# Kernel optimization log

Measured on AMD Instinct MI355X. Metric: run time of the kernel, lower is better.

Reference implementation:

```python
import jax, jax.numpy as jnp
import numpy as np
import math

L, H, E, D = 4, 8, 256, 32  # layers, heads, embed, head_dim
SCALE = 1.0 / math.sqrt(D)

def _ln(x, w, b, eps=1e-5):
    mu = jnp.mean(x, -1, keepdims=True)
    var = jnp.mean((x - mu) ** 2, -1, keepdims=True)
    return (x - mu) * jax.lax.rsqrt(var + eps) * w + b

def setup_inputs() -> dict:
    key = jax.random.key(0)
    ks = jax.random.split(key, 16)
    B, S, C = 32, 512, 512
    w = lambda k, sh: jax.random.normal(k, sh, jnp.float32) * 0.05
    return {
        'cnn_features': jax.random.normal(ks[0], (B, S, C), jnp.float32),
        'cnn_w': w(ks[1], (E, C)), 'cnn_b': jnp.zeros((E,), jnp.float32),
        'tok_emb': w(ks[2], (2, E)),
        'Wq': w(ks[3], (L, E, E)), 'bq': jnp.zeros((L, E), jnp.float32),
        'Wk': w(ks[4], (L, E, E)), 'bk': jnp.zeros((L, E), jnp.float32),
        'Wv': w(ks[5], (L, E, E)), 'bv': jnp.zeros((L, E), jnp.float32),
        'Wo': w(ks[6], (L, E, E)), 'bo': jnp.zeros((L, E), jnp.float32),
        'ln1_w': jnp.ones((L, E), jnp.float32), 'ln1_b': jnp.zeros((L, E), jnp.float32),
        'ln2_w': jnp.ones((L, E), jnp.float32), 'ln2_b': jnp.zeros((L, E), jnp.float32),
        'mlp_w1': w(ks[7], (L, 3 * E, E)), 'mlp_b1': jnp.zeros((L, 3 * E), jnp.float32),
        'mlp_w2': w(ks[8], (L, E, 3 * E)), 'mlp_b2': jnp.zeros((L, E), jnp.float32),
        'lnf_w': jnp.ones((E,), jnp.float32), 'lnf_b': jnp.zeros((E,), jnp.float32),
        'out_w1': w(ks[9], (2 * E, E)), 'out_b1': jnp.zeros((2 * E,), jnp.float32),
        'out_w2': w(ks[10], (C, 2 * E)), 'out_b2': jnp.zeros((C,), jnp.float32),
    }

def _forward(cnn_features, cnn_w, cnn_b, tok_emb, Wq, bq, Wk, bk, Wv, bv, Wo, bo,
             ln1_w, ln1_b, ln2_w, ln2_b, mlp_w1, mlp_b1, mlp_w2, mlp_b2,
             lnf_w, lnf_b, out_w1, out_b1, out_w2, out_b2):
    B, S, _ = cnn_features.shape
    # CNN feature projection + token-type embedding (all tokens type 0)
    x = cnn_features @ cnn_w.T + cnn_b + tok_emb[0]  # [B,S,E]
    for i in range(L):
        q = (x @ Wq[i].T + bq[i]).reshape(B, S, H, D).transpose(0, 2, 1, 3)
        k = (x @ Wk[i].T + bk[i]).reshape(B, S, H, D).transpose(0, 2, 1, 3)
        v = (x @ Wv[i].T + bv[i]).reshape(B, S, H, D).transpose(0, 2, 1, 3)
        scores = jnp.einsum('bhqd,bhkd->bhqk', q, k) * SCALE
        attn = jax.nn.softmax(scores, axis=-1)  # dropout = identity (eval)
        attended = jnp.einsum('bhqk,bhkd->bhqd', attn, v)
        attended = attended.transpose(0, 2, 1, 3).reshape(B, S, E)
        attn_out = attended @ Wo[i].T + bo[i]
        x = _ln(x + attn_out, ln1_w[i], ln1_b[i])
        h = jax.nn.gelu(x @ mlp_w1[i].T + mlp_b1[i], approximate=False)
        mlp_out = h @ mlp_w2[i].T + mlp_b2[i]
        x = _ln(x + mlp_out, ln2_w[i], ln2_b[i])
    x = _ln(x, lnf_w, lnf_b)
    h = jax.nn.gelu(x @ out_w1.T + out_b1, approximate=False)
    out = jax.nn.relu(h @ out_w2.T + out_b2)  # [B,S,cnn_feature_dim]
    return out

def reference(cnn_features, cnn_w, cnn_b, tok_emb, Wq, bq, Wk, bk, Wv, bv, Wo, bo,
              ln1_w, ln1_b, ln2_w, ln2_b, mlp_w1, mlp_b1, mlp_w2, mlp_b2,
              lnf_w, lnf_b, out_w1, out_b1, out_w2, out_b2):
    return _forward(cnn_features, cnn_w, cnn_b, tok_emb, Wq, bq, Wk, bk, Wv, bv, Wo, bo,
                    ln1_w, ln1_b, ln2_w, ln2_b, mlp_w1, mlp_b1, mlp_w2, mlp_b2,
                    lnf_w, lnf_b, out_w1, out_b1, out_w2, out_b2)
```

## Files before the change

### kernel.cpp

```cpp
#include <hip/hip_runtime.h>
#include <hip/hip_bf16.h>
#include <math.h>

#define B_SZ 32
#define S_SZ 512
#define C_SZ 512
#define E_SZ 256
#define H_SZ 8
#define D_SZ 32
#define L_SZ 4
#define N_TOK (B_SZ * S_SZ)
#define HID 768
#define MB (1048576)

typedef __attribute__((ext_vector_type(8))) short bf16x8;
typedef __attribute__((ext_vector_type(4))) float f32x4_t;

__device__ __forceinline__ float gelu_f(float x) {
    return 0.5f * x * (1.0f + erff(x * 0.70710678118654752f));
}

__device__ __forceinline__ ushort f2bf(float f) {
    uint u = __float_as_uint(f);
    return (ushort)((u + 0x7FFFu + ((u >> 16) & 1u)) >> 16);
}
__device__ __forceinline__ uint pack2(float a, float b) {
    __hip_bfloat162 h = __float22bfloat162_rn(make_float2(a, b));
    union { __hip_bfloat162 h; uint u; } c; c.h = h;
    return c.u;
}
__device__ __forceinline__ void unpack8(uint4 u, float* f) {
    f[0] = __uint_as_float((u.x & 0xFFFFu) << 16); f[1] = __uint_as_float(u.x & 0xFFFF0000u);
    f[2] = __uint_as_float((u.y & 0xFFFFu) << 16); f[3] = __uint_as_float(u.y & 0xFFFF0000u);
    f[4] = __uint_as_float((u.z & 0xFFFFu) << 16); f[5] = __uint_as_float(u.z & 0xFFFF0000u);
    f[6] = __uint_as_float((u.w & 0xFFFFu) << 16); f[7] = __uint_as_float(u.w & 0xFFFF0000u);
}

__device__ __forceinline__ void gload16(const ushort* g, ushort* l) {
    __builtin_amdgcn_global_load_lds(
        (const __attribute__((address_space(1))) void*)g,
        (__attribute__((address_space(3))) void*)l, 16, 0, 0);
}

__global__ __launch_bounds__(256)
void cvt_kernel(const float* __restrict__ src, ushort* __restrict__ dst)
{
    const int i = (blockIdx.x * 256 + threadIdx.x) * 8;
    const float4 a = *(const float4*)(src + i);
    const float4 b = *(const float4*)(src + i + 4);
    uint4 o;
    o.x = pack2(a.x, a.y); o.y = pack2(a.z, a.w);
    o.z = pack2(b.x, b.y); o.w = pack2(b.z, b.w);
    *(uint4*)(dst + i) = o;
}

__global__ __launch_bounds__(256)
void wqkv_cvt_kernel(const float* __restrict__ Wq, const float* __restrict__ Wk,
                     const float* __restrict__ Wv, ushort* __restrict__ dst)
{
    const int i = (blockIdx.x * 256 + threadIdx.x) * 8;
    const int layer = i / 196608;
    const int rem = i - layer * 196608;
    const int sub = rem >> 16, off = rem & 65535;
    const float* src = (sub == 0 ? Wq : sub == 1 ? Wk : Wv) + layer * 65536 + off;
    const float4 a = *(const float4*)src;
    const float4 b = *(const float4*)(src + 4);
    uint4 o;
    o.x = pack2(a.x, a.y); o.y = pack2(a.z, a.w);
    o.z = pack2(b.x, b.y); o.w = pack2(b.z, b.w);
    *(uint4*)(dst + i) = o;
}

__global__ __launch_bounds__(256)
void bqkv_kernel(const float* __restrict__ bq, const float* __restrict__ bk,
                 const float* __restrict__ bv, float* __restrict__ dst)
{
    const int idx = blockIdx.x * 256 + threadIdx.x;
    const int layer = idx / 768, j = idx % 768;
    float v = (j < 256) ? bq[layer * 256 + j]
            : (j < 512) ? bk[layer * 256 + j - 256]
                        : bv[layer * 256 + j - 512];
    dst[layer * 768 + j] = v;
}

template<int ACT, int EPI, bool OF, bool OB>
__global__ __launch_bounds__(256)
void gemm_bf16_kernel(const ushort* __restrict__ A, const ushort* __restrict__ W,
                      const float* __restrict__ bias, const float* __restrict__ bias2,
                      float* __restrict__ Cf, ushort* __restrict__ Cb,
                      ushort* __restrict__ Cb2, int M, int K, int F)
{
    __shared__ __align__(16) ushort As[2][128 * 64];
    __shared__ __align__(16) ushort Bs[2][64 * 64];
    const int tid = threadIdx.x;
    const int bm = blockIdx.x * 128, bn = blockIdx.y * 64;
    const int lane = tid & 63, w = tid >> 6;
    const int lr8 = lane >> 3, lseg = lane & 7;
    const int lsx = lseg ^ lr8;
    const int wm = w >> 1, wn = w & 1;
    const int fr = lane & 15, fk = lane >> 4;
    const int fx = fr & 7;
    f32x4_t acc[4][2] = {};

    const ushort* Ag = A + (size_t)(bm + w * 32 + lr8) * K + lsx * 8;
    const ushort* Wg = W + (size_t)(bn + w * 16 + lr8) * K + lsx * 8;

    #pragma unroll
    for (int q = 0; q < 4; ++q) gload16(Ag + (size_t)q * 8 * K, &As[0][(w * 32 + q * 8) * 64]);
    #pragma unroll
    for (int q = 0; q < 2; ++q) gload16(Wg + (size_t)q * 8 * K, &Bs[0][(w * 16 + q * 8) * 64]);
    __syncthreads();

    const int NT = K >> 6;
    int cur = 0;
    for (int t = 0; t < NT; ++t) {
        if (t + 1 < NT) {
            const size_t k0 = (size_t)(t + 1) << 6;
            #pragma unroll
            for (int q = 0; q < 4; ++q)
                gload16(Ag + (size_t)q * 8 * K + k0, &As[cur ^ 1][(w * 32 + q * 8) * 64]);
            #pragma unroll
            for (int q = 0; q < 2; ++q)
                gload16(Wg + (size_t)q * 8 * K + k0, &Bs[cur ^ 1][(w * 16 + q * 8) * 64]);
        }
        bf16x8 af[2][4], bw[2][2];
        #pragma unroll
        for (int kk = 0; kk < 2; ++kk) {
            const int rs = ((kk * 4 + fk) ^ fx) * 8;
            #pragma unroll
            for (int i = 0; i < 4; ++i)
                af[kk][i] = *(const bf16x8*)&As[cur][(wm * 64 + i * 16 + fr) * 64 + rs];
            #pragma unroll
            for (int j = 0; j < 2; ++j)
                bw[kk][j] = *(const bf16x8*)&Bs[cur][(wn * 32 + j * 16 + fr) * 64 + rs];
        }
        #pragma unroll
        for (int kk = 0; kk < 2; ++kk)
            #pragma unroll
            for (int i = 0; i < 4; ++i)
                #pragma unroll
                for (int j = 0; j < 2; ++j)
                    acc[i][j] = __builtin_amdgcn_mfma_f32_16x16x32_bf16(af[kk][i], bw[kk][j], acc[i][j], 0, 0, 0);
        __syncthreads();
        cur ^= 1;
    }

    #pragma unroll
    for (int j = 0; j < 2; ++j) {
        const int col = bn + wn * 32 + j * 16 + fr;
        float bb = bias[col];
        if (bias2) bb += bias2[col];
        #pragma unroll
        for (int i = 0; i < 4; ++i) {
            #pragma unroll
            for (int r = 0; r < 4; ++r) {
                const int row = bm + wm * 64 + i * 16 + fk * 4 + r;
                float t = acc[i][j][r] + bb;
                if (ACT == 1) t = gelu_f(t);
                if (ACT == 2) t = fmaxf(t, 0.0f);
                if (EPI == 1) {
                    const int b2 = row >> 9, s2 = row & 511;
                    if (col < 512) {
                        Cb[(size_t)row * 512 + col] = f2bf(t);
                    } else {
                        const int cc = col - 512;
                        Cb2[(size_t)(((b2 << 3) + (cc >> 5)) << 14) + ((cc & 31) << 9) + s2] = f2bf(t);
                    }
                } else {
                    if (OF) Cf[(size_t)row * F + col] = t;
                    if (OB) Cb[(size_t)row * F + col] = f2bf(t);
                }
            }
        }
    }
}

__global__ __launch_bounds__(512)
void attn_v4(const ushort* __restrict__ qk, const ushort* __restrict__ vt,
             ushort* __restrict__ out)
{
    __shared__ __align__(16) ushort Ks[512 * 40];
    __shared__ __align__(16) ushort Vs[32 * 520];
    const int bh = blockIdx.x;
    const int b = bh >> 3, h = bh & 7;
    const int tid = threadIdx.x;
    const int w = tid >> 6, lane = tid & 63;
    const int g = lane >> 4, c = lane & 15;

    #pragma unroll
    for (int i = 0; i < 4; ++i) {
        const int idx = tid + i * 512;
        const int kr = idx >> 2, seg = idx & 3;
        const uint4 kv = *(const uint4*)(qk + ((size_t)b * 512 + kr) * 512
                                         + 256 + h * 32 + seg * 8);
        const int p = (((kr >> 2) & 1) << 4) | (((kr >> 3) & 3) << 2) | (kr & 3);
        const int pos = (kr & ~31) | p;
        *(uint4*)&Ks[pos * 40 + seg * 8] = kv;
        const int dr = idx >> 6, vseg = idx & 63;
        const uint4 vv = *(const uint4*)(vt + (size_t)bh * 16384 + dr * 512 + vseg * 8);
        *(uint4*)&Vs[dr * 520 + vseg * 8] = vv;
    }

    bf16x8 qf[4];
    #pragma unroll
    for (int j = 0; j < 4; ++j) {
        const size_t qrow = (size_t)b * 512 + (j * 8 + w) * 16 + c;
        const uint4 qv = *(const uint4*)(qk + qrow * 512 + h * 32 + g * 8);
        float f[8]; unpack8(qv, f);
        const float scale = 0.17677669529663689f;
        union { uint u[4]; bf16x8 v; } qq;
        #pragma unroll
        for (int t = 0; t < 4; ++t) qq.u[t] = pack2(f[2*t] * scale, f[2*t+1] * scale);
        qf[j] = qq.v;
    }
    __syncthreads();

    const f32x4_t zz = {0.f, 0.f, 0.f, 0.f};
    #pragma unroll
    for (int j = 0; j < 4; ++j) {
        float m = -INFINITY, l = 0.f;
        f32x4_t o0 = zz, o1 = zz;
        for (int kt = 0; kt < 4; ++kt) {
            const int kbase = kt * 128;
            f32x4_t s[8];
            __builtin_amdgcn_s_setprio(1);
            #pragma unroll
            for (int kf = 0; kf < 8; ++kf) {
                const bf16x8 kfrag = *(const bf16x8*)&Ks[(kbase + kf * 16 + c) * 40 + g * 8];
                s[kf] = __builtin_amdgcn_mfma_f32_16x16x32_bf16(kfrag, qf[j], zz, 0, 0, 0);
            }
            __builtin_amdgcn_s_setprio(0);

            float mt = s[0][0];
            #pragma unroll
            for (int kf = 0; kf < 8; ++kf)
                #pragma unroll
                for (int r = 0; r < 4; ++r) mt = fmaxf(mt, s[kf][r]);
            mt = fmaxf(mt, __shfl_xor(mt, 16));
            mt = fmaxf(mt, __shfl_xor(mt, 32));
            const float mn = fmaxf(m, mt);
            const float corr = __expf(m - mn);
            m = mn;
            float lt = 0.f;
            #pragma unroll
            for (int kf = 0; kf < 8; ++kf)
                #pragma unroll
                for (int r = 0; r < 4; ++r) {
                    const float p = __expf(s[kf][r] - mn);
                    s[kf][r] = p; lt += p;
                }
            lt += __shfl_xor(lt, 16);
            lt += __shfl_xor(lt, 32);
            l = l * corr + lt;
            #pragma unroll
            for (int r = 0; r < 4; ++r) { o0[r] *= corr; o1[r] *= corr; }

            #pragma unroll
            for (int t = 0; t < 4; ++t) {
                union { uint u[4]; bf16x8 v; } pf;
                pf.u[0] = pack2(s[2*t][0],   s[2*t][1]);
                pf.u[1] = pack2(s[2*t][2],   s[2*t][3]);
                pf.u[2] = pack2(s[2*t+1][0], s[2*t+1][1]);
                pf.u[3] = pack2(s[2*t+1][2], s[2*t+1][3]);
                const bf16x8 va0 = *(const bf16x8*)&Vs[c * 520 + kbase + t * 32 + g * 8];
                const bf16x8 va1 = *(const bf16x8*)&Vs[(16 + c) * 520 + kbase + t * 32 + g * 8];
                __builtin_amdgcn_s_setprio(1);
                o0 = __builtin_amdgcn_mfma_f32_16x16x32_bf16(va0, pf.v, o0, 0, 0, 0);
                o1 = __builtin_amdgcn_mfma_f32_16x16x32_bf16(va1, pf.v, o1, 0, 0, 0);
                __builtin_amdgcn_s_setprio(0);
            }
        }

        const float inv = 1.0f / l;
        const size_t obase = ((size_t)b * 512 + (j * 8 + w) * 16 + c) * 256 + h * 32;
        ushort4 w0, w1;
        w0.x = f2bf(o0[0] * inv); w0.y = f2bf(o0[1] * inv);
        w0.z = f2bf(o0[2] * inv); w0.w = f2bf(o0[3] * inv);
        w1.x = f2bf(o1[0] * inv); w1.y = f2bf(o1[1] * inv);
        w1.z = f2bf(o1[2] * inv); w1.w = f2bf(o1[3] * inv);
        *(ushort4*)(out + obase + g * 4)      = w0;
        *(ushort4*)(out + obase + 16 + g * 4) = w1;
    }
}

__global__ __launch_bounds__(256)
void add_ln2_kernel(float* __restrict__ x, const float* __restrict__ resid,
                    const float* __restrict__ w, const float* __restrict__ b,
                    ushort* __restrict__ xb)
{
    const int lane = threadIdx.x & 63;
    const int wv = threadIdx.x >> 6;
    const size_t row = (size_t)blockIdx.x * 4 + wv;
    float4 val = *(const float4*)(x + row * E_SZ + lane * 4);
    if (resid) {
        const float4 r = *(const float4*)(resid + row * E_SZ + lane * 4);
        val.x += r.x; val.y += r.y; val.z += r.z; val.w += r.w;
    }
    float s  = val.x + val.y + val.z + val.w;
    float ss = val.x * val.x + val.y * val.y + val.z * val.z + val.w * val.w;
    #pragma unroll
    for (int off = 1; off < 64; off <<= 1) {
        s  += __shfl_xor(s, off, 64);
        ss += __shfl_xor(ss, off, 64);
    }
    const float mu  = s * (1.0f / 256.0f);
    const float var = ss * (1.0f / 256.0f) - mu * mu;
    const float rs  = rsqrtf(var + 1e-5f);
    const float4 wv4 = *(const float4*)(w + lane * 4);
    const float4 bv4 = *(const float4*)(b + lane * 4);
    float4 o;
    o.x = (val.x - mu) * rs * wv4.x + bv4.x;
    o.y = (val.y - mu) * rs * wv4.y + bv4.y;
    o.z = (val.z - mu) * rs * wv4.z + bv4.z;
    o.w = (val.w - mu) * rs * wv4.w + bv4.w;
    *(float4*)(x + row * E_SZ + lane * 4) = o;
    ushort4 ob;
    ob.x = f2bf(o.x); ob.y = f2bf(o.y); ob.z = f2bf(o.z); ob.w = f2bf(o.w);
    *(ushort4*)(xb + row * E_SZ + lane * 4) = ob;
}

extern "C" void kernel_launch(void* const* d_in, const int* in_sizes, int n_in,
                              void* d_out, int out_size, void* d_ws, size_t ws_size,
                              hipStream_t stream)
{
    const float* cnn   = (const float*)d_in[0];
    const float* cnn_w = (const float*)d_in[1];
    const float* cnn_b = (const float*)d_in[2];
    const float* tok   = (const float*)d_in[3];
    const float* Wq    = (const float*)d_in[4];
    const float* bq    = (const float*)d_in[5];
    const float* Wk    = (const float*)d_in[6];
    const float* bk    = (const float*)d_in[7];
    const float* Wv    = (const float*)d_in[8];
    const float* bv    = (const float*)d_in[9];
    const float* Wo    = (const float*)d_in[10];
    const float* bo    = (const float*)d_in[11];
    const float* ln1w  = (const float*)d_in[12];
    const float* ln1b  = (const float*)d_in[13];
    const float* ln2w  = (const float*)d_in[14];
    const float* ln2b  = (const float*)d_in[15];
    const float* mw1   = (const float*)d_in[16];
    const float* mb1   = (const float*)d_in[17];
    const float* mw2   = (const float*)d_in[18];
    const float* mb2   = (const float*)d_in[19];
    const float* lnfw  = (const float*)d_in[20];
    const float* lnfb  = (const float*)d_in[21];
    const float* ow1   = (const float*)d_in[22];
    const float* ob1   = (const float*)d_in[23];
    const float* ow2   = (const float*)d_in[24];
    const float* ob2   = (const float*)d_in[25];

    const int M = N_TOK;
    char* ws = (char*)d_ws;

    float*  x     = (float*)(ws + 0);
    ushort* xb    = (ushort*)(ws + 16 * MB);
    ushort* qkb   = (ushort*)(ws + 24 * MB);
    float*  resid = (float*)(ws + 24 * MB);
    ushort* cnnb  = (ushort*)(ws + 24 * MB);
    ushort* vt    = (ushort*)(ws + 40 * MB);
    ushort* ab_   = (ushort*)(ws + 48 * MB);
    ushort* hb_   = (ushort*)(ws + 40 * MB);
    ushort* wb    = (ushort*)(ws + 64 * MB);

    ushort* cnn_wb = wb;
    ushort* Wob    = wb + 131072;
    ushort* wqkv   = wb + 393216;
    ushort* mw1b   = wb + 1179648;
    ushort* mw2b   = wb + 1966080;
    ushort* ow1b   = wb + 2752512;
    ushort* ow2b   = wb + 2883584;
    float*  bqkv   = (float*)(ws + 64 * MB + 6291456);

    cvt_kernel<<<dim3(4096), dim3(256), 0, stream>>>(cnn, cnnb);
    cvt_kernel<<<dim3(64),  dim3(256), 0, stream>>>(cnn_w, cnn_wb);
    cvt_kernel<<<dim3(128), dim3(256), 0, stream>>>(Wo, Wob);
    cvt_kernel<<<dim3(384), dim3(256), 0, stream>>>(mw1, mw1b);
    cvt_kernel<<<dim3(384), dim3(256), 0, stream>>>(mw2, mw2b);
    cvt_kernel<<<dim3(64),  dim3(256), 0, stream>>>(ow1, ow1b);
    cvt_kernel<<<dim3(128), dim3(256), 0, stream>>>(ow2, ow2b);
    wqkv_cvt_kernel<<<dim3(384), dim3(256), 0, stream>>>(Wq, Wk, Wv, wqkv);
    bqkv_kernel<<<dim3(12), dim3(256), 0, stream>>>(bq, bk, bv, bqkv);

    gemm_bf16_kernel<0, 0, true, true><<<dim3(M / 128, E_SZ / 64), dim3(256), 0, stream>>>(
        cnnb, cnn_wb, cnn_b, tok, x, xb, nullptr, M, C_SZ, E_SZ);

    for (int i = 0; i < L_SZ; ++i) {
        gemm_bf16_kernel<0, 1, false, false><<<dim3(M / 128, HID / 64), dim3(256), 0, stream>>>(
            xb, wqkv + (size_t)i * 196608, bqkv + (size_t)i * 768, nullptr,
            nullptr, qkb, vt, M, E_SZ, HID);

        attn_v4<<<dim3(B_SZ * H_SZ), dim3(512), 0, stream>>>(qkb, vt, ab_);

        gemm_bf16_kernel<0, 0, true, false><<<dim3(M / 128, E_SZ / 64), dim3(256), 0, stream>>>(
            ab_, Wob + (size_t)i * 65536, bo + (size_t)i * E_SZ, nullptr,
            resid, nullptr, nullptr, M, E_SZ, E_SZ);
        add_ln2_kernel<<<dim3(M / 4), dim3(256), 0, stream>>>(
            x, resid, ln1w + (size_t)i * E_SZ, ln1b + (size_t)i * E_SZ, xb);

        gemm_bf16_kernel<1, 0, false, true><<<dim3(M / 128, HID / 64), dim3(256), 0, stream>>>(
            xb, mw1b + (size_t)i * HID * E_SZ, mb1 + (size_t)i * HID, nullptr,
            nullptr, hb_, nullptr, M, E_SZ, HID);
        gemm_bf16_kernel<0, 0, true, false><<<dim3(M / 128, E_SZ / 64), dim3(256), 0, stream>>>(
            hb_, mw2b + (size_t)i * E_SZ * HID, mb2 + (size_t)i * E_SZ, nullptr,
            resid, nullptr, nullptr, M, HID, E_SZ);
        add_ln2_kernel<<<dim3(M / 4), dim3(256), 0, stream>>>(
            x, resid, ln2w + (size_t)i * E_SZ, ln2b + (size_t)i * E_SZ, xb);
    }

    add_ln2_kernel<<<dim3(M / 4), dim3(256), 0, stream>>>(x, nullptr, lnfw, lnfb, xb);

    gemm_bf16_kernel<1, 0, false, true><<<dim3(M / 128, (2 * E_SZ) / 64), dim3(256), 0, stream>>>(
        xb, ow1b, ob1, nullptr, nullptr, hb_, nullptr, M, E_SZ, 2 * E_SZ);
    gemm_bf16_kernel<2, 0, true, false><<<dim3(M / 128, C_SZ / 64), dim3(256), 0, stream>>>(
        hb_, ow2b, ob2, nullptr, (float*)d_out, nullptr, nullptr, M, 2 * E_SZ, C_SZ);
}
```

Baseline: 578.8 us.

## Fuse residual add and LayerNorm into output-projection and MLP-down GEMMs

Adds a GEMM kernel in which each block owns a full 64x256 row tile, so it can add bias and residual and compute LayerNorm in the epilogue. This removes the fp32 resid buffer round trip and the separate add+LN kernels (8 launches) inside the layer loop. The final LN kernel no longer writes fp32 x back. It also merges the seven weight-conversion launches into one kernel. The cost is fewer blocks (256 instead of 512) with a wider N tile per block, and a cross-wave reduction through LDS.

```diff
diff --git a/kernel.cpp b/kernel.cpp
--- a/kernel.cpp
+++ b/kernel.cpp
@@ -55,20 +55,32 @@
 }
 
 __global__ __launch_bounds__(256)
-void wqkv_cvt_kernel(const float* __restrict__ Wq, const float* __restrict__ Wk,
-                     const float* __restrict__ Wv, ushort* __restrict__ dst)
+void wcvt_kernel(const float* __restrict__ cnn_w, const float* __restrict__ Wo,
+                 const float* __restrict__ Wq, const float* __restrict__ Wk,
+                 const float* __restrict__ Wv, const float* __restrict__ mw1,
+                 const float* __restrict__ mw2, const float* __restrict__ ow1,
+                 const float* __restrict__ ow2, ushort* __restrict__ wb)
 {
     const int i = (blockIdx.x * 256 + threadIdx.x) * 8;
-    const int layer = i / 196608;
-    const int rem = i - layer * 196608;
-    const int sub = rem >> 16, off = rem & 65535;
-    const float* src = (sub == 0 ? Wq : sub == 1 ? Wk : Wv) + layer * 65536 + off;
+    const float* src;
+    if (i < 131072)       src = cnn_w + i;
+    else if (i < 393216)  src = Wo + (i - 131072);
+    else if (i < 1179648) {
+        const int r = i - 393216;
+        const int layer = r / 196608, rem = r % 196608;
+        const int sub = rem >> 16, off = rem & 65535;
+        src = (sub == 0 ? Wq : sub == 1 ? Wk : Wv) + layer * 65536 + off;
+    }
+    else if (i < 1966080) src = mw1 + (i - 1179648);
+    else if (i < 2752512) src = mw2 + (i - 1966080);
+    else if (i < 2883584) src = ow1 + (i - 2752512);
+    else                  src = ow2 + (i - 2883584);
     const float4 a = *(const float4*)src;
     const float4 b = *(const float4*)(src + 4);
     uint4 o;
     o.x = pack2(a.x, a.y); o.y = pack2(a.z, a.w);
     o.z = pack2(b.x, b.y); o.w = pack2(b.z, b.w);
-    *(uint4*)(dst + i) = o;
+    *(uint4*)(wb + i) = o;
 }
 
 __global__ __launch_bounds__(256)
@@ -176,6 +188,120 @@
 }
 
 __global__ __launch_bounds__(512)
+void gemm_ln_kernel(const ushort* __restrict__ A, const ushort* __restrict__ W,
+                    const float* __restrict__ bias, float* __restrict__ x,
+                    ushort* __restrict__ xb, const float* __restrict__ lnw,
+                    const float* __restrict__ lnb, int K)
+{
+    __shared__ __align__(16) ushort As[2][64 * 64];
+    __shared__ __align__(16) ushort Bs[2][256 * 64];
+    __shared__ float psum[64][8], psq[64][8], murs[64][2];
+    const int tid = threadIdx.x;
+    const int bm = blockIdx.x * 64;
+    const int lane = tid & 63, w = tid >> 6;
+    const int lr8 = lane >> 3, lseg = lane & 7;
+    const int lsx = lseg ^ lr8;
+    const int fr = lane & 15, fk = lane >> 4;
+    const int fx = fr & 7;
+    f32x4_t acc[4][2] = {};
+
+    const ushort* Ag = A + (size_t)(bm + w * 8 + lr8) * K + lsx * 8;
+    const ushort* Wg = W + (size_t)(w * 32 + lr8) * K + lsx * 8;
+
+    gload16(Ag, &As[0][(w * 8) * 64]);
+    #pragma unroll
+    for (int q = 0; q < 4; ++q) gload16(Wg + (size_t)q * 8 * K, &Bs[0][(w * 32 + q * 8) * 64]);
+    __syncthreads();
+
+    const int NT = K >> 6;
+    int cur = 0;
+    for (int t = 0; t < NT; ++t) {
+        if (t + 1 < NT) {
+            const size_t k0 = (size_t)(t + 1) << 6;
+            gload16(Ag + k0, &As[cur ^ 1][(w * 8) * 64]);
+            #pragma unroll
+            for (int q = 0; q < 4; ++q)
+                gload16(Wg + (size_t)q * 8 * K + k0, &Bs[cur ^ 1][(w * 32 + q * 8) * 64]);
+        }
+        bf16x8 af[2][4], bw[2][2];
+        #pragma unroll
+        for (int kk = 0; kk < 2; ++kk) {
+            const int rs = ((kk * 4 + fk) ^ fx) * 8;
+            #pragma unroll
+            for (int i = 0; i < 4; ++i)
+                af[kk][i] = *(const bf16x8*)&As[cur][(i * 16 + fr) * 64 + rs];
+            #pragma unroll
+            for (int j = 0; j < 2; ++j)
+                bw[kk][j] = *(const bf16x8*)&Bs[cur][(w * 32 + j * 16 + fr) * 64 + rs];
+        }
+        #pragma unroll
+        for (int kk = 0; kk < 2; ++kk)
+            #pragma unroll
+            for (int i = 0; i < 4; ++i)
+                #pragma unroll
+                for (int j = 0; j < 2; ++j)
+                    acc[i][j] = __builtin_amdgcn_mfma_f32_16x16x32_bf16(af[kk][i], bw[kk][j], acc[i][j], 0, 0, 0);
+        __syncthreads();
+        cur ^= 1;
+    }
+
+    float y[4][2][4];
+    #pragma unroll
+    for (int j = 0; j < 2; ++j) {
+        const int col = w * 32 + j * 16 + fr;
+        const float bb = bias[col];
+        #pragma unroll
+        for (int i = 0; i < 4; ++i)
+            #pragma unroll
+            for (int r = 0; r < 4; ++r) {
+                const int row = i * 16 + fk * 4 + r;
+                y[i][j][r] = acc[i][j][r] + bb + x[(size_t)(bm + row) * 256 + col];
+            }
+    }
+    #pragma unroll
+    for (int i = 0; i < 4; ++i)
+        #pragma unroll
+        for (int r = 0; r < 4; ++r) {
+            float s = y[i][0][r] + y[i][1][r];
+            float q = y[i][0][r] * y[i][0][r] + y[i][1][r] * y[i][1][r];
+            #pragma unroll
+            for (int off = 1; off < 16; off <<= 1) {
+                s += __shfl_xor(s, off);
+                q += __shfl_xor(q, off);
+            }
+            if (fr == 0) {
+                psum[i * 16 + fk * 4 + r][w] = s;
+                psq [i * 16 + fk * 4 + r][w] = q;
+            }
+        }
+    __syncthreads();
+    if (tid < 64) {
+        float ms = 0.f, mq = 0.f;
+        #pragma unroll
+        for (int ww = 0; ww < 8; ++ww) { ms += psum[tid][ww]; mq += psq[tid][ww]; }
+        const float mu = ms * (1.0f / 256.0f);
+        const float var = mq * (1.0f / 256.0f) - mu * mu;
+        murs[tid][0] = mu;
+        murs[tid][1] = rsqrtf(var + 1e-5f);
+    }
+    __syncthreads();
+    #pragma unroll
+    for (int i = 0; i < 4; ++i)
+        #pragma unroll
+        for (int r = 0; r < 4; ++r) {
+            const int row = i * 16 + fk * 4 + r;
+            const float mu = murs[row][0], rs = murs[row][1];
+            #pragma unroll
+            for (int j = 0; j < 2; ++j) {
+                const int col = w * 32 + j * 16 + fr;
+                const float xn = (y[i][j][r] - mu) * rs * lnw[col] + lnb[col];
+                x [(size_t)(bm + row) * 256 + col] = xn;
+                xb[(size_t)(bm + row) * 256 + col] = f2bf(xn);
+            }
+        }
+}
+
+__global__ __launch_bounds__(512)
 void attn_v4(const ushort* __restrict__ qk, const ushort* __restrict__ vt,
              ushort* __restrict__ out)
 {
@@ -284,18 +410,13 @@
 }
 
 __global__ __launch_bounds__(256)
-void add_ln2_kernel(float* __restrict__ x, const float* __restrict__ resid,
-                    const float* __restrict__ w, const float* __restrict__ b,
-                    ushort* __restrict__ xb)
+void lnf_kernel(const float* __restrict__ x, const float* __restrict__ w,
+                const float* __restrict__ b, ushort* __restrict__ xb)
 {
     const int lane = threadIdx.x & 63;
     const int wv = threadIdx.x >> 6;
     const size_t row = (size_t)blockIdx.x * 4 + wv;
-    float4 val = *(const float4*)(x + row * E_SZ + lane * 4);
-    if (resid) {
-        const float4 r = *(const float4*)(resid + row * E_SZ + lane * 4);
-        val.x += r.x; val.y += r.y; val.z += r.z; val.w += r.w;
-    }
+    const float4 val = *(const float4*)(x + row * E_SZ + lane * 4);
     float s  = val.x + val.y + val.z + val.w;
     float ss = val.x * val.x + val.y * val.y + val.z * val.z + val.w * val.w;
     #pragma unroll
@@ -308,14 +429,11 @@
     const float rs  = rsqrtf(var + 1e-5f);
     const float4 wv4 = *(const float4*)(w + lane * 4);
     const float4 bv4 = *(const float4*)(b + lane * 4);
-    float4 o;
-    o.x = (val.x - mu) * rs * wv4.x + bv4.x;
-    o.y = (val.y - mu) * rs * wv4.y + bv4.y;
-    o.z = (val.z - mu) * rs * wv4.z + bv4.z;
-    o.w = (val.w - mu) * rs * wv4.w + bv4.w;
-    *(float4*)(x + row * E_SZ + lane * 4) = o;
     ushort4 ob;
-    ob.x = f2bf(o.x); ob.y = f2bf(o.y); ob.z = f2bf(o.z); ob.w = f2bf(o.w);
+    ob.x = f2bf((val.x - mu) * rs * wv4.x + bv4.x);
+    ob.y = f2bf((val.y - mu) * rs * wv4.y + bv4.y);
+    ob.z = f2bf((val.z - mu) * rs * wv4.z + bv4.z);
+    ob.w = f2bf((val.w - mu) * rs * wv4.w + bv4.w);
     *(ushort4*)(xb + row * E_SZ + lane * 4) = ob;
 }
 
@@ -356,7 +474,6 @@
     float*  x     = (float*)(ws + 0);
     ushort* xb    = (ushort*)(ws + 16 * MB);
     ushort* qkb   = (ushort*)(ws + 24 * MB);
-    float*  resid = (float*)(ws + 24 * MB);
     ushort* cnnb  = (ushort*)(ws + 24 * MB);
     ushort* vt    = (ushort*)(ws + 40 * MB);
     ushort* ab_   = (ushort*)(ws + 48 * MB);
@@ -373,13 +490,8 @@
     float*  bqkv   = (float*)(ws + 64 * MB + 6291456);
 
     cvt_kernel<<<dim3(4096), dim3(256), 0, stream>>>(cnn, cnnb);
-    cvt_kernel<<<dim3(64),  dim3(256), 0, stream>>>(cnn_w, cnn_wb);
-    cvt_kernel<<<dim3(128), dim3(256), 0, stream>>>(Wo, Wob);
-    cvt_kernel<<<dim3(384), dim3(256), 0, stream>>>(mw1, mw1b);
-    cvt_kernel<<<dim3(384), dim3(256), 0, stream>>>(mw2, mw2b);
-    cvt_kernel<<<dim3(64),  dim3(256), 0, stream>>>(ow1, ow1b);
-    cvt_kernel<<<dim3(128), dim3(256), 0, stream>>>(ow2, ow2b);
-    wqkv_cvt_kernel<<<dim3(384), dim3(256), 0, stream>>>(Wq, Wk, Wv, wqkv);
+    wcvt_kernel<<<dim3(1536), dim3(256), 0, stream>>>(
+        cnn_w, Wo, Wq, Wk, Wv, mw1, mw2, ow1, ow2, wb);
     bqkv_kernel<<<dim3(12), dim3(256), 0, stream>>>(bq, bk, bv, bqkv);
 
     gemm_bf16_kernel<0, 0, true, true><<<dim3(M / 128, E_SZ / 64), dim3(256), 0, stream>>>(
@@ -392,23 +504,20 @@
 
         attn_v4<<<dim3(B_SZ * H_SZ), dim3(512), 0, stream>>>(qkb, vt, ab_);
 
-        gemm_bf16_kernel<0, 0, true, false><<<dim3(M / 128, E_SZ / 64), dim3(256), 0, stream>>>(
-            ab_, Wob + (size_t)i * 65536, bo + (size_t)i * E_SZ, nullptr,
-            resid, nullptr, nullptr, M, E_SZ, E_SZ);
-        add_ln2_kernel<<<dim3(M / 4), dim3(256), 0, stream>>>(
-            x, resid, ln1w + (size_t)i * E_SZ, ln1b + (size_t)i * E_SZ, xb);
+        gemm_ln_kernel<<<dim3(M / 64), dim3(512), 0, stream>>>(
+            ab_, Wob + (size_t)i * 65536, bo + (size_t)i * E_SZ,
+            x, xb, ln1w + (size_t)i * E_SZ, ln1b + (size_t)i * E_SZ, E_SZ);
 
         gemm_bf16_kernel<1, 0, false, true><<<dim3(M / 128, HID / 64), dim3(256), 0, stream>>>(
             xb, mw1b + (size_t)i * HID * E_SZ, mb1 + (size_t)i * HID, nullptr,
             nullptr, hb_, nullptr, M, E_SZ, HID);
-        gemm_bf16_kernel<0, 0, true, false><<<dim3(M / 128, E_SZ / 64), dim3(256), 0, stream>>>(
-            hb_, mw2b + (size_t)i * E_SZ * HID, mb2 + (size_t)i * E_SZ, nullptr,
-            resid, nullptr, nullptr, M, HID, E_SZ);
-        add_ln2_kernel<<<dim3(M / 4), dim3(256), 0, stream>>>(
-            x, resid, ln2w + (size_t)i * E_SZ, ln2b + (size_t)i * E_SZ, xb);
-    }
-
-    add_ln2_kernel<<<dim3(M / 4), dim3(256), 0, stream>>>(x, nullptr, lnfw, lnfb, xb);
+
+        gemm_ln_kernel<<<dim3(M / 64), dim3(512), 0, stream>>>(
+            hb_, mw2b + (size_t)i * E_SZ * HID, mb2 + (size_t)i * E_SZ,
+            x, xb, ln2w + (size_t)i * E_SZ, ln2b + (size_t)i * E_SZ, HID);
+    }
+
+    lnf_kernel<<<dim3(M / 4), dim3(256), 0, stream>>>(x, lnfw, lnfb, xb);
 
     gemm_bf16_kernel<1, 0, false, true><<<dim3(M / 128, (2 * E_SZ) / 64), dim3(256), 0, stream>>>(
         xb, ow1b, ob1, nullptr, nullptr, hb_, nullptr, M, E_SZ, 2 * E_SZ);
```

Result: faster. 522.7 us (-9.7%).
